# Performance work log

Hardware: AMD Instinct MI355X
Metric: run time of the kernel (lower is better)

The kernel has to match this reference:

```python
import jax, jax.numpy as jnp
import numpy as np

D = 1024
EPS = 1e-5

def layer_norm(x, g, b):
    m = jnp.mean(x, axis=-1, keepdims=True)
    v = jnp.mean(jnp.square(x - m), axis=-1, keepdims=True)
    return (x - m) * jax.lax.rsqrt(v + EPS) * g + b

def setup_inputs() -> dict:
    key = jax.random.key(0)
    ks = jax.random.split(key, 8)
    S, B = 4096, 4
    s = 1.0 / np.sqrt(D)
    return {
        "x": jax.random.normal(ks[0], (S, B, D), dtype=jnp.float32),
        "W_v": jax.random.uniform(ks[1], (D, D), jnp.float32, -s, s),
        "theta": jax.random.uniform(ks[2], (D, D), jnp.float32, -s, s),
        "ln1_g": jnp.ones((D,), jnp.float32),
        "ln1_b": jnp.zeros((D,), jnp.float32),
        "ln2_g": jnp.ones((D,), jnp.float32),
        "ln2_b": jnp.zeros((D,), jnp.float32),
        "w1": jax.random.uniform(ks[3], (4 * D, D), jnp.float32, -s, s),
        "b1": jnp.zeros((4 * D,), jnp.float32),
        "w2": jax.random.uniform(ks[4], (D, 4 * D), jnp.float32, -1.0 / np.sqrt(4 * D), 1.0 / np.sqrt(4 * D)),
        "b2": jnp.zeros((D,), jnp.float32),
    }

def reference(x, W_v, theta, ln1_g, ln1_b, ln2_g, ln2_b, w1, b1, w2, b2):
    # x: [S, B, D]
    h = layer_norm(x, ln1_g, ln1_b)
    X = jnp.transpose(h, (1, 0, 2))          # [B, n, D], n = S
    n = X.shape[1]
    XWv = X @ W_v.T                          # [B, n, D]
    Xth = X @ theta.T                        # [B, n, D]
    # first term: (1/n) * ones(n,n) @ XWv == seq-mean broadcast over rows
    first = jnp.mean(XWv, axis=1, keepdims=True)
    # second term reassociated: (X @ theta(X)^T) @ XWv == X @ (theta(X)^T @ XWv)
    M = jnp.einsum('bnd,bne->bde', Xth, XWv)  # [B, D, D]
    second = (1.0 / (n * np.sqrt(D))) * jnp.einsum('bnd,bde->bne', X, M)
    attn = first + second                    # [B, n, D]
    X = X + attn
    h = jnp.transpose(X, (1, 0, 2))          # [S, B, D]
    h2 = layer_norm(h, ln2_g, ln2_b)
    mlp = jax.nn.gelu(h2 @ w1.T + b1, approximate=False) @ w2.T + b2
    return h + mlp
```

## Files before the change

kernel.cpp:

```cpp
#include <hip/hip_runtime.h>
#include <math.h>

#define S_ 4096
#define B_ 4
#define D_ 1024
#define R_ (S_*B_)
#define H_ (4*D_)

typedef unsigned short u16;
typedef unsigned int   u32;
typedef __attribute__((ext_vector_type(8))) short bf16x8;
typedef __attribute__((ext_vector_type(4))) float f32x4;

__device__ __forceinline__ u16 f2bf(float f) {
  u32 u = __float_as_uint(f);
  u32 r = (u + 0x7fffu + ((u >> 16) & 1u)) >> 16;
  return (u16)r;
}
__device__ __forceinline__ float bf2f(u16 u) {
  return __uint_as_float(((u32)u) << 16);
}

__device__ __forceinline__ void gl_lds16(const u16* g, u16* l) {
  __builtin_amdgcn_global_load_lds((const __attribute__((address_space(1))) void*)g,
                                   (__attribute__((address_space(3))) void*)l,
                                   16, 0, 0);
}
__device__ __forceinline__ void BAR() {
  asm volatile("s_barrier" ::: "memory");
}

__global__ __launch_bounds__(256) void f2bf_k(const float* __restrict__ in,
                                              u16* __restrict__ out, int n4) {
  int i = blockIdx.x * 256 + threadIdx.x;
  if (i < n4) {
    float4 v = ((const float4*)in)[i];
    ushort4 o = make_ushort4(f2bf(v.x), f2bf(v.y), f2bf(v.z), f2bf(v.w));
    ((ushort4*)out)[i] = o;
  }
}

template<bool TR>
__global__ __launch_bounds__(256) void ln_k(const float* __restrict__ x,
                                            u16* __restrict__ o,
                                            const float* __restrict__ g,
                                            const float* __restrict__ bb) {
  const int row = blockIdx.x;
  const int tid = threadIdx.x;
  const float4 v = *(const float4*)&x[(long)row * D_ + tid * 4];
  float vv[4] = {v.x, v.y, v.z, v.w};
  float s = vv[0] + vv[1] + vv[2] + vv[3];
  float q = vv[0]*vv[0] + vv[1]*vv[1] + vv[2]*vv[2] + vv[3]*vv[3];
  const int l = tid & 63, w = tid >> 6;
  #pragma unroll
  for (int off = 32; off > 0; off >>= 1) {
    s += __shfl_down(s, off, 64);
    q += __shfl_down(q, off, 64);
  }
  __shared__ float red[8];
  if (l == 0) { red[w] = s; red[4 + w] = q; }
  __syncthreads();
  s = red[0] + red[1] + red[2] + red[3];
  q = red[4] + red[5] + red[6] + red[7];
  const float m   = s * (1.0f / D_);
  const float var = q * (1.0f / D_) - m * m;
  const float inv = rsqrtf(var + 1e-5f);
  const long orow = TR ? ((long)(row % B_) * S_ + (row / B_)) : (long)row;
  const int j = tid * 4;
  ushort4 ou = make_ushort4(
      f2bf((vv[0] - m) * inv * g[j+0] + bb[j+0]),
      f2bf((vv[1] - m) * inv * g[j+1] + bb[j+1]),
      f2bf((vv[2] - m) * inv * g[j+2] + bb[j+2]),
      f2bf((vv[3] - m) * inv * g[j+3] + bb[j+3]));
  *(ushort4*)&o[orow * D_ + j] = ou;
}

__global__ __launch_bounds__(256) void colsum_k(const u16* __restrict__ Xw,
                                                float* __restrict__ first) {
  const int d  = blockIdx.x * 256 + threadIdx.x;
  const int b  = blockIdx.z;
  const int n0 = blockIdx.y * 256;
  const u16* p = Xw + ((long)b * S_ + n0) * D_ + d;
  float s = 0.f;
  #pragma unroll 8
  for (int n = 0; n < 256; ++n) s += bf2f(p[(long)n * D_]);
  atomicAdd(&first[b * D_ + d], s);
}

__global__ __launch_bounds__(256) void tr_k(const u16* __restrict__ in,
                                            u16* __restrict__ out) {
  __shared__ u16 t[64][65];
  const int b  = blockIdx.z;
  const int e0 = blockIdx.x * 64;
  const int n0 = blockIdx.y * 64;
  const int tid = threadIdx.x;
  #pragma unroll
  for (int i = 0; i < 4; ++i) {
    const int v = i * 256 + tid;
    const int r = v >> 4;
    const int c = (v & 15) << 2;
    ushort4 d4 = *(const ushort4*)&in[((long)b * S_ + n0 + r) * D_ + e0 + c];
    t[r][c+0] = d4.x; t[r][c+1] = d4.y; t[r][c+2] = d4.z; t[r][c+3] = d4.w;
  }
  __syncthreads();
  #pragma unroll
  for (int i = 0; i < 4; ++i) {
    const int v = i * 256 + tid;
    const int e = v >> 4;
    const int c = (v & 15) << 2;
    ushort4 o4 = make_ushort4(t[c+0][e], t[c+1][e], t[c+2][e], t[c+3][e]);
    *(ushort4*)&out[((long)b * D_ + e0 + e) * S_ + n0 + c] = o4;
  }
}

template<int EPI>
__global__ __launch_bounds__(256, 2) void gemm_k(
    const u16* __restrict__ A, long sAz,
    const u16* __restrict__ B, long sBz,
    int K, int ldc,
    u16* __restrict__ Cb, long sCz,
    float* __restrict__ Cf,
    const float* __restrict__ vec1,
    float scale)
{
  const int bz = blockIdx.z;
  const u16* Ab = A + (long)bz * sAz;
  const u16* Bb = B + (long)bz * sBz;
  const int row0 = blockIdx.x * 128;
  const int col0 = blockIdx.y * 128;
  const int lda = K;

  __shared__ __align__(16) u16 As[128 * 32];
  __shared__ __align__(16) u16 Bs[128 * 32];

  const int tid = threadIdx.x;
  const int w = tid >> 6;
  const int l = tid & 63;
  const int wr = (w >> 1) * 64;
  const int wc = (w & 1) * 64;

  f32x4 acc[4][4];
  #pragma unroll
  for (int mi = 0; mi < 4; ++mi)
    #pragma unroll
    for (int ni = 0; ni < 4; ++ni) acc[mi][ni] = (f32x4){0.f, 0.f, 0.f, 0.f};

  const int lrow = l & 15;
  const int lo   = l >> 4;

  for (int k0 = 0; k0 < K; k0 += 32) {
    __syncthreads();
    #pragma unroll
    for (int it = 0; it < 2; ++it) {
      const int cb = it * 256 + (w << 6);
      const int c  = cb + l;
      const int r  = c >> 2;
      const int qs = ((c & 3) ^ ((r >> 1) & 3)) << 3;
      gl_lds16(Ab + (long)(row0 + r) * lda + (k0 + qs), &As[cb << 3]);
      gl_lds16(Bb + (long)(col0 + r) * lda + (k0 + qs), &Bs[cb << 3]);
    }
    __syncthreads();

    bf16x8 af[4], bfr[4];
    #pragma unroll
    for (int mi = 0; mi < 4; ++mi) {
      const int R = wr + mi * 16 + lrow;
      af[mi]  = *(const bf16x8*)&As[R * 32 + ((lo ^ ((R >> 1) & 3)) << 3)];
    }
    #pragma unroll
    for (int ni = 0; ni < 4; ++ni) {
      const int R = wc + ni * 16 + lrow;
      bfr[ni] = *(const bf16x8*)&Bs[R * 32 + ((lo ^ ((R >> 1) & 3)) << 3)];
    }
    #pragma unroll
    for (int mi = 0; mi < 4; ++mi)
      #pragma unroll
      for (int ni = 0; ni < 4; ++ni)
        acc[mi][ni] = __builtin_amdgcn_mfma_f32_16x16x32_bf16(af[mi], bfr[ni], acc[mi][ni], 0, 0, 0);
  }

  const int rbase = row0 + wr + (lo << 2);
  const int cbase = col0 + wc + lrow;
  #pragma unroll
  for (int mi = 0; mi < 4; ++mi)
    #pragma unroll
    for (int ni = 0; ni < 4; ++ni)
      #pragma unroll
      for (int r = 0; r < 4; ++r) {
        const int i = rbase + mi * 16 + r;
        const int j = cbase + ni * 16;
        if constexpr (EPI == 0)
          Cb[(long)bz * sCz + (long)i * ldc + j] = f2bf(acc[mi][ni][r]);
      }
  (void)Cf; (void)vec1; (void)scale;
}

template<int EPI>
__global__ __launch_bounds__(512, 2) void gemm256_k(
    const u16* __restrict__ A, long sAz,
    const u16* __restrict__ B, long sBz,
    int K, int ldc,
    u16* __restrict__ Cb, long sCz,
    float* __restrict__ Cf,
    const float* __restrict__ vec1,
    float scale)
{
  const int bz = blockIdx.z;
  const u16* Ab = A + (long)bz * sAz;
  const u16* Bb = B + (long)bz * sBz;
  const int row0 = blockIdx.x * 256;
  const int col0 = blockIdx.y * 256;

  __shared__ __align__(16) u16 As[2][256 * 64];
  __shared__ __align__(16) u16 Bs[2][256 * 64];

  const int tid = threadIdx.x;
  const int w   = tid >> 6;
  const int l   = tid & 63;
  const int wm  = w >> 2;
  const int wn  = w & 3;
  const int lr  = l & 15;
  const int lo  = l >> 4;

  const int rstage = w * 32 + (l >> 3);
  const int qst    = ((l & 7) ^ (l >> 3)) << 3;

  const int qa0 = ((0 + lo) ^ (lr & 7)) << 3;
  const int qa1 = ((4 + lo) ^ (lr & 7)) << 3;

  f32x4 acc[8][4];
  #pragma unroll
  for (int mi = 0; mi < 8; ++mi)
    #pragma unroll
    for (int ni = 0; ni < 4; ++ni) acc[mi][ni] = (f32x4){0.f, 0.f, 0.f, 0.f};

  const int NT = K >> 6;

  auto STAGE = [&](int tn, int buf) {
    const long ko = (long)tn * 64;
    const u16* asrc = Ab + (long)(row0 + rstage) * K + ko + qst;
    const u16* bsrc = Bb + (long)(col0 + rstage) * K + ko + qst;
    u16* ald = &As[buf][(w * 4) * 512];
    u16* bld = &Bs[buf][(w * 4) * 512];
    #pragma unroll
    for (int i = 0; i < 4; ++i) {
      gl_lds16(asrc + (long)(i * 8) * K, ald + i * 512);
      gl_lds16(bsrc + (long)(i * 8) * K, bld + i * 512);
    }
  };

  STAGE(0, 0);
  __syncthreads();

  for (int t = 0; t < NT; ++t) {
    const int cur = t & 1;
    const u16* Ac = As[cur];
    const u16* Bc = Bs[cur];
    bf16x8 af[4], bf[4];

    #pragma unroll
    for (int ni = 0; ni < 4; ++ni)
      bf[ni] = *(const bf16x8*)&Bc[(wn * 64 + ni * 16 + lr) * 64 + qa0];
    #pragma unroll
    for (int mi = 0; mi < 4; ++mi)
      af[mi] = *(const bf16x8*)&Ac[(wm * 128 + mi * 16 + lr) * 64 + qa0];
    if (t + 1 < NT) STAGE(t + 1, cur ^ 1);
    BAR();
    __builtin_amdgcn_s_setprio(1);
    #pragma unroll
    for (int mi = 0; mi < 4; ++mi)
      #pragma unroll
      for (int ni = 0; ni < 4; ++ni)
        acc[mi][ni] = __builtin_amdgcn_mfma_f32_16x16x32_bf16(af[mi], bf[ni], acc[mi][ni], 0, 0, 0);
    __builtin_amdgcn_s_setprio(0);
    BAR();

    #pragma unroll
    for (int mi = 0; mi < 4; ++mi)
      af[mi] = *(const bf16x8*)&Ac[(wm * 128 + 64 + mi * 16 + lr) * 64 + qa0];
    BAR();
    __builtin_amdgcn_s_setprio(1);
    #pragma unroll
    for (int mi = 0; mi < 4; ++mi)
      #pragma unroll
      for (int ni = 0; ni < 4; ++ni)
        acc[4 + mi][ni] = __builtin_amdgcn_mfma_f32_16x16x32_bf16(af[mi], bf[ni], acc[4 + mi][ni], 0, 0, 0);
    __builtin_amdgcn_s_setprio(0);
    BAR();

    #pragma unroll
    for (int ni = 0; ni < 4; ++ni)
      bf[ni] = *(const bf16x8*)&Bc[(wn * 64 + ni * 16 + lr) * 64 + qa1];
    #pragma unroll
    for (int mi = 0; mi < 4; ++mi)
      af[mi] = *(const bf16x8*)&Ac[(wm * 128 + mi * 16 + lr) * 64 + qa1];
    BAR();
    __builtin_amdgcn_s_setprio(1);
    #pragma unroll
    for (int mi = 0; mi < 4; ++mi)
      #pragma unroll
      for (int ni = 0; ni < 4; ++ni)
        acc[mi][ni] = __builtin_amdgcn_mfma_f32_16x16x32_bf16(af[mi], bf[ni], acc[mi][ni], 0, 0, 0);
    __builtin_amdgcn_s_setprio(0);
    BAR();

    #pragma unroll
    for (int mi = 0; mi < 4; ++mi)
      af[mi] = *(const bf16x8*)&Ac[(wm * 128 + 64 + mi * 16 + lr) * 64 + qa1];
    BAR();
    __builtin_amdgcn_s_setprio(1);
    #pragma unroll
    for (int mi = 0; mi < 4; ++mi)
      #pragma unroll
      for (int ni = 0; ni < 4; ++ni)
        acc[4 + mi][ni] = __builtin_amdgcn_mfma_f32_16x16x32_bf16(af[mi], bf[ni], acc[4 + mi][ni], 0, 0, 0);
    __builtin_amdgcn_s_setprio(0);
    asm volatile("s_waitcnt vmcnt(0)" ::: "memory");
    BAR();
  }

  const int rbase = row0 + wm * 128 + (lo << 2);
  const int cbase = col0 + wn * 64 + lr;
  #pragma unroll
  for (int mi = 0; mi < 8; ++mi) {
    #pragma unroll
    for (int ni = 0; ni < 4; ++ni) {
      #pragma unroll
      for (int r = 0; r < 4; ++r) {
        const int i = rbase + mi * 16 + r;
        const int j = cbase + ni * 16;
        const float a = acc[mi][ni][r];
        if constexpr (EPI == 0) {
          Cb[(long)bz * sCz + (long)i * ldc + j] = f2bf(a);
        } else if constexpr (EPI == 1) {
          const float xv = bf2f(Ab[(long)i * K + j]);
          Cf[((long)i * B_ + bz) * (long)D_ + j] =
              xv + vec1[bz * D_ + j] * (1.0f / S_) + scale * a;
        } else if constexpr (EPI == 2) {
          const float tt = a + vec1[j];
          const float ge = 0.5f * tt * (1.0f + erff(tt * 0.70710678118654752f));
          Cb[(long)i * ldc + j] = f2bf(ge);
        } else {
          const long idx = (long)i * ldc + j;
          Cf[idx] = Cf[idx] + a + vec1[j];
        }
      }
    }
  }
}

extern "C" void kernel_launch(void* const* d_in, const int* in_sizes, int n_in,
                              void* d_out, int out_size, void* d_ws, size_t ws_size,
                              hipStream_t stream) {
  (void)in_sizes; (void)n_in; (void)out_size; (void)ws_size;
  const float* x     = (const float*)d_in[0];
  const float* W_v   = (const float*)d_in[1];
  const float* theta = (const float*)d_in[2];
  const float* ln1g  = (const float*)d_in[3];
  const float* ln1b  = (const float*)d_in[4];
  const float* ln2g  = (const float*)d_in[5];
  const float* ln2b  = (const float*)d_in[6];
  const float* w1    = (const float*)d_in[7];
  const float* b1    = (const float*)d_in[8];
  const float* w2    = (const float*)d_in[9];
  const float* b2    = (const float*)d_in[10];
  float* out = (float*)d_out;

  char* ws = (char*)d_ws;
  const size_t MB = 1024ull * 1024ull;
  const size_t KB = 1024ull;
  u16*   Wv_bf = (u16*)(ws + 0);
  u16*   Th_bf = (u16*)(ws + 2 * MB);
  u16*   w1_bf = (u16*)(ws + 4 * MB);
  u16*   w2_bf = (u16*)(ws + 12 * MB);
  float* first = (float*)(ws + 20 * MB);
  u16*   Mt    = (u16*)(ws + 21 * MB);
  u16*   Xn    = (u16*)(ws + 29 * MB);
  u16*   XWv   = (u16*)(ws + 61 * MB);
  u16*   Xth   = (u16*)(ws + 93 * MB);
  u16*   XWvT  = (u16*)(ws + 125 * MB);
  u16*   XthT  = (u16*)(ws + 157 * MB);
  u16*   h2    = (u16*)(ws + 29 * MB);
  u16*   G     = (u16*)(ws + 61 * MB);
  (void)KB;

  f2bf_k<<<dim3((D_*D_/4 + 255)/256), 256, 0, stream>>>(W_v,   Wv_bf, D_*D_/4);
  f2bf_k<<<dim3((D_*D_/4 + 255)/256), 256, 0, stream>>>(theta, Th_bf, D_*D_/4);
  f2bf_k<<<dim3((H_*D_/4 + 255)/256), 256, 0, stream>>>(w1,    w1_bf, H_*D_/4);
  f2bf_k<<<dim3((H_*D_/4 + 255)/256), 256, 0, stream>>>(w2,    w2_bf, H_*D_/4);

  ln_k<true><<<dim3(R_), 256, 0, stream>>>(x, Xn, ln1g, ln1b);

  gemm256_k<0><<<dim3(R_/256, D_/256, 2), 512, 0, stream>>>(
      Xn, 0, Wv_bf, (long)D_*D_, D_, D_, XWv, (long)R_*D_, nullptr, nullptr, 0.f);

  hipMemsetAsync(first, 0, B_ * D_ * sizeof(float), stream);
  colsum_k<<<dim3(D_/256, 16, B_), 256, 0, stream>>>(XWv, first);

  tr_k<<<dim3(D_/64, S_/64, B_), 256, 0, stream>>>(XWv, XWvT);
  tr_k<<<dim3(D_/64, S_/64, B_), 256, 0, stream>>>(Xth, XthT);

  gemm_k<0><<<dim3(D_/128, D_/128, B_), 256, 0, stream>>>(
      XWvT, (long)D_*S_, XthT, (long)D_*S_, S_, D_, Mt, (long)D_*D_, nullptr, nullptr, 0.f);

  gemm256_k<1><<<dim3(S_/256, D_/256, B_), 512, 0, stream>>>(
      Xn, (long)S_*D_, Mt, (long)D_*D_, D_, D_, nullptr, 0, out, first,
      1.0f / ((float)S_ * 32.0f));

  ln_k<false><<<dim3(R_), 256, 0, stream>>>(out, h2, ln2g, ln2b);

  gemm256_k<2><<<dim3(R_/256, H_/256, 1), 512, 0, stream>>>(
      h2, 0, w1_bf, 0, D_, H_, G, 0, nullptr, b1, 0.f);
  gemm256_k<3><<<dim3(R_/256, D_/256, 1), 512, 0, stream>>>(
      G, 0, w2_bf, 0, H_, D_, nullptr, 0, out, b2, 0.f);
}
```

Baseline: 625.2 us.

## Deepen GEMM K-pipeline with half-tile LDS stages and tanh-form GELU

```diff
diff --git a/kernel.cpp b/kernel.cpp
--- a/kernel.cpp
+++ b/kernel.cpp
@@ -28,6 +28,11 @@
 }
 __device__ __forceinline__ void BAR() {
   asm volatile("s_barrier" ::: "memory");
+}
+
+__device__ __forceinline__ float gelu_f(float t) {
+  const float u2 = 1.5957691216f * t + 0.0713548162726f * t * t * t;
+  return t / (1.0f + __expf(-u2));
 }
 
 __global__ __launch_bounds__(256) void f2bf_k(const float* __restrict__ in,
@@ -211,8 +216,7 @@
   const int row0 = blockIdx.x * 256;
   const int col0 = blockIdx.y * 256;
 
-  __shared__ __align__(16) u16 As[2][256 * 64];
-  __shared__ __align__(16) u16 Bs[2][256 * 64];
+  __shared__ __align__(16) u16 Lds[2][2][2][256 * 32];
 
   const int tid = threadIdx.x;
   const int w   = tid >> 6;
@@ -222,11 +226,21 @@
   const int lr  = l & 15;
   const int lo  = l >> 4;
 
-  const int rstage = w * 32 + (l >> 3);
-  const int qst    = ((l & 7) ^ (l >> 3)) << 3;
-
-  const int qa0 = ((0 + lo) ^ (lr & 7)) << 3;
-  const int qa1 = ((4 + lo) ^ (lr & 7)) << 3;
+  const int NKH = K >> 5;
+  const int NT  = K >> 6;
+
+  const int rs   = w * 32 + (l >> 2);
+  const int qsrc = ((l & 3) ^ ((l >> 3) & 3)) << 3;
+
+  const int qsw = (lo ^ ((lr >> 1) & 3)) << 3;
+
+  auto STAGE = [&](int khg, int op) {
+    if (khg >= NKH) return;
+    const u16* src = (op ? Bb : Ab) + (long)((op ? col0 : row0) + rs) * K + khg * 32 + qsrc;
+    u16* dst = &Lds[(khg >> 1) & 1][khg & 1][op][(w * 2) * 512];
+    gl_lds16(src, dst);
+    gl_lds16(src + (long)16 * K, dst + 512);
+  };
 
   f32x4 acc[8][4];
   #pragma unroll
@@ -234,37 +248,26 @@
     #pragma unroll
     for (int ni = 0; ni < 4; ++ni) acc[mi][ni] = (f32x4){0.f, 0.f, 0.f, 0.f};
 
-  const int NT = K >> 6;
-
-  auto STAGE = [&](int tn, int buf) {
-    const long ko = (long)tn * 64;
-    const u16* asrc = Ab + (long)(row0 + rstage) * K + ko + qst;
-    const u16* bsrc = Bb + (long)(col0 + rstage) * K + ko + qst;
-    u16* ald = &As[buf][(w * 4) * 512];
-    u16* bld = &Bs[buf][(w * 4) * 512];
-    #pragma unroll
-    for (int i = 0; i < 4; ++i) {
-      gl_lds16(asrc + (long)(i * 8) * K, ald + i * 512);
-      gl_lds16(bsrc + (long)(i * 8) * K, bld + i * 512);
-    }
-  };
-
-  STAGE(0, 0);
-  __syncthreads();
-
-  for (int t = 0; t < NT; ++t) {
-    const int cur = t & 1;
-    const u16* Ac = As[cur];
-    const u16* Bc = Bs[cur];
+  STAGE(0, 0); STAGE(0, 1);
+  STAGE(1, 0); STAGE(1, 1);
+  STAGE(2, 0); STAGE(2, 1);
+  asm volatile("s_waitcnt vmcnt(8)" ::: "memory");
+  BAR();
+
+  for (int kt = 0; kt < NT; ++kt) {
+    const u16* L00 = &Lds[kt & 1][0][0][0];
+    const u16* L01 = &Lds[kt & 1][0][1][0];
+    const u16* L10 = &Lds[kt & 1][1][0][0];
+    const u16* L11 = &Lds[kt & 1][1][1][0];
     bf16x8 af[4], bf[4];
 
     #pragma unroll
     for (int ni = 0; ni < 4; ++ni)
-      bf[ni] = *(const bf16x8*)&Bc[(wn * 64 + ni * 16 + lr) * 64 + qa0];
-    #pragma unroll
-    for (int mi = 0; mi < 4; ++mi)
-      af[mi] = *(const bf16x8*)&Ac[(wm * 128 + mi * 16 + lr) * 64 + qa0];
-    if (t + 1 < NT) STAGE(t + 1, cur ^ 1);
+      bf[ni] = *(const bf16x8*)&L01[(wn * 64 + ni * 16 + lr) * 32 + qsw];
+    #pragma unroll
+    for (int mi = 0; mi < 4; ++mi)
+      af[mi] = *(const bf16x8*)&L00[(wm * 128 + mi * 16 + lr) * 32 + qsw];
+    STAGE(2 * kt + 3, 0);
     BAR();
     __builtin_amdgcn_s_setprio(1);
     #pragma unroll
@@ -277,7 +280,10 @@
 
     #pragma unroll
     for (int mi = 0; mi < 4; ++mi)
-      af[mi] = *(const bf16x8*)&Ac[(wm * 128 + 64 + mi * 16 + lr) * 64 + qa0];
+      af[mi] = *(const bf16x8*)&L00[(wm * 128 + 64 + mi * 16 + lr) * 32 + qsw];
+    STAGE(2 * kt + 3, 1);
+    if (kt == NT - 1) asm volatile("s_waitcnt vmcnt(0)" ::: "memory");
+    else              asm volatile("s_waitcnt vmcnt(8)" ::: "memory");
     BAR();
     __builtin_amdgcn_s_setprio(1);
     #pragma unroll
@@ -290,10 +296,11 @@
 
     #pragma unroll
     for (int ni = 0; ni < 4; ++ni)
-      bf[ni] = *(const bf16x8*)&Bc[(wn * 64 + ni * 16 + lr) * 64 + qa1];
-    #pragma unroll
-    for (int mi = 0; mi < 4; ++mi)
-      af[mi] = *(const bf16x8*)&Ac[(wm * 128 + mi * 16 + lr) * 64 + qa1];
+      bf[ni] = *(const bf16x8*)&L11[(wn * 64 + ni * 16 + lr) * 32 + qsw];
+    #pragma unroll
+    for (int mi = 0; mi < 4; ++mi)
+      af[mi] = *(const bf16x8*)&L10[(wm * 128 + mi * 16 + lr) * 32 + qsw];
+    STAGE(2 * kt + 4, 0);
     BAR();
     __builtin_amdgcn_s_setprio(1);
     #pragma unroll
@@ -306,7 +313,11 @@
 
     #pragma unroll
     for (int mi = 0; mi < 4; ++mi)
-      af[mi] = *(const bf16x8*)&Ac[(wm * 128 + 64 + mi * 16 + lr) * 64 + qa1];
+      af[mi] = *(const bf16x8*)&L10[(wm * 128 + 64 + mi * 16 + lr) * 32 + qsw];
+    STAGE(2 * kt + 4, 1);
+    if (kt < NT - 2)       asm volatile("s_waitcnt vmcnt(8)" ::: "memory");
+    else if (kt == NT - 2) asm volatile("s_waitcnt vmcnt(4)" ::: "memory");
+    else                   asm volatile("s_waitcnt vmcnt(0)" ::: "memory");
     BAR();
     __builtin_amdgcn_s_setprio(1);
     #pragma unroll
@@ -315,7 +326,6 @@
       for (int ni = 0; ni < 4; ++ni)
         acc[4 + mi][ni] = __builtin_amdgcn_mfma_f32_16x16x32_bf16(af[mi], bf[ni], acc[4 + mi][ni], 0, 0, 0);
     __builtin_amdgcn_s_setprio(0);
-    asm volatile("s_waitcnt vmcnt(0)" ::: "memory");
     BAR();
   }
 
@@ -337,9 +347,7 @@
           Cf[((long)i * B_ + bz) * (long)D_ + j] =
               xv + vec1[bz * D_ + j] * (1.0f / S_) + scale * a;
         } else if constexpr (EPI == 2) {
-          const float tt = a + vec1[j];
-          const float ge = 0.5f * tt * (1.0f + erff(tt * 0.70710678118654752f));
-          Cb[(long)i * ldc + j] = f2bf(ge);
+          Cb[(long)i * ldc + j] = f2bf(gelu_f(a + vec1[j]));
         } else {
           const long idx = (long)i * ldc + j;
           Cf[idx] = Cf[idx] + a + vec1[j];
@@ -368,7 +376,6 @@
 
   char* ws = (char*)d_ws;
   const size_t MB = 1024ull * 1024ull;
-  const size_t KB = 1024ull;
   u16*   Wv_bf = (u16*)(ws + 0);
   u16*   Th_bf = (u16*)(ws + 2 * MB);
   u16*   w1_bf = (u16*)(ws + 4 * MB);
@@ -382,7 +389,6 @@
   u16*   XthT  = (u16*)(ws + 157 * MB);
   u16*   h2    = (u16*)(ws + 29 * MB);
   u16*   G     = (u16*)(ws + 61 * MB);
-  (void)KB;
 
   f2bf_k<<<dim3((D_*D_/4 + 255)/256), 256, 0, stream>>>(W_v,   Wv_bf, D_*D_/4);
   f2bf_k<<<dim3((D_*D_/4 + 255)/256), 256, 0, stream>>>(theta, Th_bf, D_*D_/4);
```

New measurement: 607.1 us. 1.03x faster.
